# Kernel tuning notes

Hardware: AMD Instinct MI355X
Metric: run time of the kernel (lower is better)

Reference implementation:

```python
import jax, jax.numpy as jnp
import numpy as np

VOCAB, EMB, HID = 50000, 256, 512
H = HID // 2            # per-direction hidden size
K = 24                  # tagset size
START, STOP = 22, 23
B, T = 32, 512
NEG = -10000.0


def setup_inputs():
    key = jax.random.key(0)
    ks = jax.random.split(key, 16)
    s = 0.1  # weight scale to keep gates in a sane range
    sentence = jax.random.randint(ks[0], (B, T), 0, VOCAB)
    embedding = jax.random.normal(ks[1], (VOCAB, EMB), jnp.float32)
    w_ih_f = jax.random.normal(ks[2], (4 * H, EMB), jnp.float32) * s
    w_hh_f = jax.random.normal(ks[3], (4 * H, H), jnp.float32) * s
    b_ih_f = jax.random.normal(ks[4], (4 * H,), jnp.float32) * s
    b_hh_f = jax.random.normal(ks[5], (4 * H,), jnp.float32) * s
    w_ih_b = jax.random.normal(ks[6], (4 * H, EMB), jnp.float32) * s
    w_hh_b = jax.random.normal(ks[7], (4 * H, H), jnp.float32) * s
    b_ih_b = jax.random.normal(ks[8], (4 * H,), jnp.float32) * s
    b_hh_b = jax.random.normal(ks[9], (4 * H,), jnp.float32) * s
    w_out = jax.random.normal(ks[10], (K, HID), jnp.float32) * s
    b_out = jax.random.normal(ks[11], (K,), jnp.float32) * s
    transitions = jax.random.normal(ks[12], (K, K), jnp.float32)
    transitions = transitions.at[START, :].set(NEG).at[:, STOP].set(NEG)
    h0 = jax.random.normal(ks[13], (2, B, H), jnp.float32)  # [fwd,bwd] initial h
    c0 = jax.random.normal(ks[14], (2, B, H), jnp.float32)  # [fwd,bwd] initial c
    return {"sentence": sentence, "embedding": embedding,
            "w_ih_f": w_ih_f, "w_hh_f": w_hh_f, "b_ih_f": b_ih_f, "b_hh_f": b_hh_f,
            "w_ih_b": w_ih_b, "w_hh_b": w_hh_b, "b_ih_b": b_ih_b, "b_hh_b": b_hh_b,
            "w_out": w_out, "b_out": b_out, "transitions": transitions,
            "h0": h0, "c0": c0}


def _lstm_dir(x_tbe, w_ih, w_hh, b_ih, b_hh, h0, c0, reverse):
    # x_tbe: [T, B, E]; PyTorch gate order i, f, g, o
    def step(carry, x_t):
        h, c = carry
        gates = x_t @ w_ih.T + b_ih + h @ w_hh.T + b_hh  # [B, 4H]
        i, f, g, o = jnp.split(gates, 4, axis=-1)
        c = jax.nn.sigmoid(f) * c + jax.nn.sigmoid(i) * jnp.tanh(g)
        h = jax.nn.sigmoid(o) * jnp.tanh(c)
        return (h, c), h
    _, hs = jax.lax.scan(step, (h0, c0), x_tbe, reverse=reverse)
    return hs  # [T, B, H]


def _viterbi(feats_tbk, transitions):
    # feats_tbk: [T, B, K]; transitions[next, prev]
    init = jnp.full((B, K), NEG, feats_tbk.dtype).at[:, START].set(0.0)

    def step(fv, feat_t):
        scores = fv[:, None, :] + transitions[None, :, :]  # [B, next, prev]
        bp = jnp.argmax(scores, axis=-1)                   # [B, K]
        fv_new = jnp.max(scores, axis=-1) + feat_t
        return fv_new, bp

    fv, bps = jax.lax.scan(step, init, feats_tbk)  # bps: [T, B, K]
    terminal = fv + transitions[STOP][None, :]
    last_tag = jnp.argmax(terminal, axis=-1)       # [B]
    path_score = jnp.max(terminal, axis=-1)        # [B]

    def back(tag, bp_t):
        prev = jnp.take_along_axis(bp_t, tag[:, None], axis=1)[:, 0]
        return prev, tag
    # process t = T-1 .. 0; carry holds tag at time t, emits it, steps to t-1
    _, path = jax.lax.scan(back, last_tag, bps, reverse=True)  # [T, B]
    return path_score, path.T.astype(jnp.int32)  # [B], [B, T]


def reference(sentence, embedding, w_ih_f, w_hh_f, b_ih_f, b_hh_f,
              w_ih_b, w_hh_b, b_ih_b, b_hh_b, w_out, b_out,
              transitions, h0, c0):
    emb = embedding[sentence]                       # [B, T, EMB]
    x = jnp.transpose(emb, (1, 0, 2))               # [T, B, EMB]
    hf = _lstm_dir(x, w_ih_f, w_hh_f, b_ih_f, b_hh_f, h0[0], c0[0], False)
    hb = _lstm_dir(x, w_ih_b, w_hh_b, b_ih_b, b_hh_b, h0[1], c0[1], True)
    hs = jnp.concatenate([hf, hb], axis=-1)         # [T, B, HID]
    feats = hs @ w_out.T + b_out                    # [T, B, K]
    score, path = _viterbi(feats, transitions)
    return score, path
```

## Files before the change

kernel.cpp:

```cpp
#include <hip/hip_runtime.h>

#define T_LEN 512
#define BATCH 32
#define HDIR  256
#define KTAG  24
#define START_TAG 22
#define STOP_TAG  23
#define NEGV  (-10000.0f)
#define SENTU 0x7FC0DEADu

typedef float vf4 __attribute__((ext_vector_type(4)));

#define XPROJ_OFF   0ull
#define XPROJ_ELEMS (2ull*512*1024*32)
#define FEATS_OFF   (XPROJ_OFF + XPROJ_ELEMS)
#define FEATS_ELEMS (512ull*32*24)
#define HIST_OFF    (FEATS_OFF + FEATS_ELEMS)
#define HIST_ELEMS  (2ull*513*8192)

#define BARRIER_LGKM() asm volatile("s_waitcnt lgkmcnt(0)\n\ts_barrier" ::: "memory")

__device__ __forceinline__ float fsig(float x) {
  return __builtin_amdgcn_rcpf(1.0f + __expf(-x));
}
__device__ __forceinline__ float ftanh(float x) {
  return 2.0f * __builtin_amdgcn_rcpf(1.0f + __expf(-2.0f * x)) - 1.0f;
}
__device__ __forceinline__ unsigned um(unsigned a, unsigned b) { return a < b ? a : b; }
__device__ __forceinline__ float rdlane(float v, int l) {
  return __uint_as_float((unsigned)__builtin_amdgcn_readlane((int)__float_as_uint(v), l));
}

__global__ void k_fill(float* __restrict__ p, int n4) {
  int i = blockIdx.x * blockDim.x + threadIdx.x;
  if (i < n4) {
    float* dst = p + (size_t)i * 4;
    const float sv = __uint_as_float(SENTU);
    vf4 v; v.x = sv; v.y = sv; v.z = sv; v.w = sv;
    asm volatile("global_store_dwordx4 %0, %1, off sc0 sc1"
                 :: "v"(dst), "v"(v) : "memory");
  }
}

__global__ __launch_bounds__(256, 1) void k_main(
    const int* __restrict__ sent, const float* __restrict__ emb,
    const float* __restrict__ wihf, const float* __restrict__ wihb,
    const float* __restrict__ bihf, const float* __restrict__ bhhf,
    const float* __restrict__ bihb, const float* __restrict__ bhhb,
    const float* __restrict__ whhf, const float* __restrict__ whhb,
    const float* __restrict__ h0, const float* __restrict__ c0,
    const float* __restrict__ wout, const float* __restrict__ bout,
    float* __restrict__ xproj, float* __restrict__ feats,
    float* __restrict__ hist)
{
  extern __shared__ float dynpad[];
  __shared__ float smem[12544];
  const int bid = blockIdx.x;
  const int tid = threadIdx.x;
  if (sent == (const int*)0) dynpad[0] = 0.f;

  if (bid >= 64 && bid < 2112) {
    float (*As)[132] = (float (*)[132])(smem);
    float (*Bs)[132] = (float (*)[132])(smem + 2112);
    int* sid = (int*)(smem + 4224);
    const int idx = bid - 64;
    const int mt_rank = idx >> 4;
    const int sub = idx & 15;
    const int y = sub >> 1;
    const int dir = sub & 1;
    const int mt = (mt_rank & 1) ? (127 - (mt_rank >> 1)) : (mt_rank >> 1);
    const int m0 = mt * 128;
    const int n0 = y * 128;
    const float* __restrict__ W = dir ? wihb : wihf;
    if (tid < 128) {
      int m = m0 + tid;
      sid[tid] = sent[(m & 31) * 512 + (m >> 5)];
    }
    __syncthreads();
    float acc[8][8];
#pragma unroll
    for (int i = 0; i < 8; ++i)
#pragma unroll
      for (int j = 0; j < 8; ++j) acc[i][j] = 0.f;
    const int r = tid >> 1, qq = tid & 1;
    const int ty = tid >> 4, tx = tid & 15;
    const float* ap = &emb[(size_t)sid[r] * 256 + qq * 8];
    const float* bp = &W[(size_t)(n0 + r) * 256 + qq * 8];
    float4 a0 = *(const float4*)(ap);
    float4 a1 = *(const float4*)(ap + 4);
    float4 b0 = *(const float4*)(bp);
    float4 b1 = *(const float4*)(bp + 4);
    for (int k0 = 0; k0 < 256; k0 += 16) {
      __syncthreads();
      As[qq*8+0][r] = a0.x; As[qq*8+1][r] = a0.y; As[qq*8+2][r] = a0.z; As[qq*8+3][r] = a0.w;
      As[qq*8+4][r] = a1.x; As[qq*8+5][r] = a1.y; As[qq*8+6][r] = a1.z; As[qq*8+7][r] = a1.w;
      Bs[qq*8+0][r] = b0.x; Bs[qq*8+1][r] = b0.y; Bs[qq*8+2][r] = b0.z; Bs[qq*8+3][r] = b0.w;
      Bs[qq*8+4][r] = b1.x; Bs[qq*8+5][r] = b1.y; Bs[qq*8+6][r] = b1.z; Bs[qq*8+7][r] = b1.w;
      __syncthreads();
      if (k0 + 16 < 256) {
        const float* ap2 = ap + k0 + 16;
        const float* bp2 = bp + k0 + 16;
        a0 = *(const float4*)(ap2);
        a1 = *(const float4*)(ap2 + 4);
        b0 = *(const float4*)(bp2);
        b1 = *(const float4*)(bp2 + 4);
      }
#pragma unroll
      for (int kk = 0; kk < 16; ++kk) {
        float4 av0 = *(const float4*)&As[kk][ty*8];
        float4 av1 = *(const float4*)&As[kk][ty*8+4];
        float4 bv0 = *(const float4*)&Bs[kk][tx*8];
        float4 bv1 = *(const float4*)&Bs[kk][tx*8+4];
        float am[8] = {av0.x,av0.y,av0.z,av0.w,av1.x,av1.y,av1.z,av1.w};
        float bn[8] = {bv0.x,bv0.y,bv0.z,bv0.w,bv1.x,bv1.y,bv1.z,bv1.w};
#pragma unroll
        for (int i = 0; i < 8; ++i)
#pragma unroll
          for (int j = 0; j < 8; ++j)
            acc[i][j] = fmaf(am[i], bn[j], acc[i][j]);
      }
    }
    const float* bi_p = dir ? bihb : bihf;
    const float* bh_p = dir ? bhhb : bhhf;
    float bias[8];
#pragma unroll
    for (int j = 0; j < 8; ++j) { int n = n0 + tx*8 + j; bias[j] = bi_p[n] + bh_p[n]; }
    const int mb = m0 + ty * 8;
    const int tt = mb >> 5, bb = mb & 31;
#pragma unroll
    for (int j = 0; j < 8; ++j) {
      int n = n0 + tx*8 + j;
      float* dst = &xproj[((((size_t)dir*512 + tt)*1024) + n)*32 + bb];
      vf4 o0, o1;
      o0[0] = acc[0][j]+bias[j]; o0[1] = acc[1][j]+bias[j];
      o0[2] = acc[2][j]+bias[j]; o0[3] = acc[3][j]+bias[j];
      o1[0] = acc[4][j]+bias[j]; o1[1] = acc[5][j]+bias[j];
      o1[2] = acc[6][j]+bias[j]; o1[3] = acc[7][j]+bias[j];
      asm volatile(
        "global_store_dwordx4 %0, %2, off sc0 sc1\n\t"
        "global_store_dwordx4 %1, %3, off sc0 sc1"
        :: "v"(dst), "v"(dst + 4), "v"(o0), "v"(o1) : "memory");
    }
    asm volatile("s_waitcnt vmcnt(0)" ::: "memory");
    __syncthreads();
    if (tid == 0) {
      float* fp = hist + (size_t)dir * 1024 + (size_t)mt * 8 + y;
      const float z = 0.f;
      asm volatile("global_store_dword %0, %1, off sc0 sc1"
                   :: "v"(fp), "v"(z) : "memory");
    }
    return;
  }

  if (bid >= 2112) {
    const int f = bid - 2112;
    const int t = (f & 1) ? (256 + (f >> 1)) : (255 - (f >> 1));
    float* hlds = smem;
    const float* sF = hist + ((size_t)0*513 + (t + 1)) * 8192;
    const float* sB = hist + ((size_t)1*513 + (512 - t)) * 8192;
    {
      const int p = tid & 31;
      const float* pp = (((tid >> 5) & 1) ? sB : sF) + 32 * p;
      while (true) {
        float v;
        asm volatile("global_load_dword %0, %1, off sc0 sc1\n\ts_waitcnt vmcnt(0)"
                     : "=&v"(v) : "v"(pp) : "memory");
        int bad = (__float_as_uint(v) == SENTU) ? 1 : 0;
        if (!__any(bad)) break;
        __builtin_amdgcn_s_sleep(64);
      }
    }
    const int b = tid >> 3, ks = tid & 7;
    float accv[3];
    for (int dir2 = 0; dir2 < 2; ++dir2) {
      const float* sp = (dir2 ? sB : sF) + (size_t)tid * 4;
      vf4 v[8];
      while (true) {
        asm volatile(
          "global_load_dwordx4 %0, %8, off sc0 sc1\n\t"
          "global_load_dwordx4 %1, %9, off sc0 sc1\n\t"
          "global_load_dwordx4 %2, %10, off sc0 sc1\n\t"
          "global_load_dwordx4 %3, %11, off sc0 sc1\n\t"
          "global_load_dwordx4 %4, %12, off sc0 sc1\n\t"
          "global_load_dwordx4 %5, %13, off sc0 sc1\n\t"
          "global_load_dwordx4 %6, %14, off sc0 sc1\n\t"
          "global_load_dwordx4 %7, %15, off sc0 sc1\n\t"
          "s_waitcnt vmcnt(0)"
          : "=&v"(v[0]), "=&v"(v[1]), "=&v"(v[2]), "=&v"(v[3]),
            "=&v"(v[4]), "=&v"(v[5]), "=&v"(v[6]), "=&v"(v[7])
          : "v"(sp), "v"(sp+1024), "v"(sp+2048), "v"(sp+3072),
            "v"(sp+4096), "v"(sp+5120), "v"(sp+6144), "v"(sp+7168)
          : "memory");
        unsigned z = 0xFFFFFFFFu;
#pragma unroll
        for (int q = 0; q < 8; ++q)
#pragma unroll
          for (int bl = 0; bl < 4; ++bl)
            z = um(z, __float_as_uint(v[q][bl]) ^ SENTU);
        if (z) break;
        __builtin_amdgcn_s_sleep(16);
      }
#pragma unroll
      for (int q = 0; q < 8; ++q)
#pragma unroll
        for (int bl = 0; bl < 4; ++bl)
          hlds[(4*q + bl)*258 + tid] = v[q][bl];
      __syncthreads();
#pragma unroll
      for (int kt = 0; kt < 3; ++kt) {
        const int k = kt * 8 + ks;
        if (dir2 == 0) accv[kt] = bout[k];
        const float* wr = wout + (size_t)k * 512 + dir2 * 256;
        float a = accv[kt];
#pragma unroll 8
        for (int kk = 0; kk < 256; kk += 4) {
          float4 h4 = *(const float4*)&hlds[b * 258 + kk];
          float4 w4 = *(const float4*)&wr[kk];
          a += h4.x*w4.x + h4.y*w4.y + h4.z*w4.z + h4.w*w4.w;
        }
        accv[kt] = a;
      }
      __syncthreads();
    }
#pragma unroll
    for (int kt = 0; kt < 3; ++kt)
      feats[((size_t)t * 32 + b) * 24 + kt * 8 + ks] = accv[kt];
    return;
  }

  float* hl = smem + 4352;
  const int dir = bid >> 5;
  const int slice = bid & 31;
  const int rowg = tid >> 5;
  const int bgrp = (tid >> 3) & 3;
  const int kgrp = tid & 7;
  const int jg = slice * 8 + rowg;
  const float* __restrict__ W = dir ? whhb : whhf;

  float2 w2[4][16];
#pragma unroll
  for (int g = 0; g < 4; ++g)
#pragma unroll
    for (int kk2 = 0; kk2 < 16; ++kk2)
      w2[g][kk2] = *(const float2*)&W[(size_t)(g*256 + jg)*256 + kgrp*32 + 2*kk2];

  float cc[8];
#pragma unroll
  for (int bi = 0; bi < 8; ++bi)
    cc[bi] = c0[(size_t)(dir*32 + bgrp*8 + bi)*256 + jg];

  const int kk = tid & 31;
  const int base_col = tid & ~31;
  const int kw4 = 4*((tid >> 5) & 7);
  const int rot = (4*kgrp + 2*bgrp) & 31;
  float* const histd = hist + (size_t)dir * 513 * 8192;
  float hnew[8];

  for (int s = 0; s < 512; ++s) {
    const int t = dir ? (511 - s) : s;

    vf4 hv[8];
    if (s == 0) {
#pragma unroll
      for (int q = 0; q < 8; ++q)
#pragma unroll
        for (int bl = 0; bl < 4; ++bl)
          hv[q][bl] = h0[(size_t)(dir*32 + 4*q + bl)*256 + tid];
    } else {
      const float* sp = histd + (size_t)s*8192 + (size_t)tid*4;
      const float* p0 = sp;
      const float* p1 = sp + 1024;
      const float* p2 = sp + 2048;
      const float* p3 = sp + 3072;
      const float* p4 = sp + 4096;
      const float* p5 = sp + 5120;
      const float* p6 = sp + 6144;
      const float* p7 = sp + 7168;
      while (true) {
        asm volatile(
          "global_load_dwordx4 %0, %1, off sc0 sc1\n\t"
          "s_waitcnt vmcnt(0)"
          : "=&v"(hv[7]) : "v"(p7) : "memory");
        unsigned z = 0xFFFFFFFFu;
#pragma unroll
        for (int bl = 0; bl < 4; ++bl)
          z = um(z, __float_as_uint(hv[7][bl]) ^ SENTU);
        if (z) break;
        __builtin_amdgcn_s_sleep(1);
      }
      while (true) {
        asm volatile(
          "global_load_dwordx4 %0, %7, off sc0 sc1\n\t"
          "global_load_dwordx4 %1, %8, off sc0 sc1\n\t"
          "global_load_dwordx4 %2, %9, off sc0 sc1\n\t"
          "global_load_dwordx4 %3, %10, off sc0 sc1\n\t"
          "global_load_dwordx4 %4, %11, off sc0 sc1\n\t"
          "global_load_dwordx4 %5, %12, off sc0 sc1\n\t"
          "global_load_dwordx4 %6, %13, off sc0 sc1\n\t"
          "s_waitcnt vmcnt(0)"
          : "=&v"(hv[0]), "=&v"(hv[1]), "=&v"(hv[2]), "=&v"(hv[3]),
            "=&v"(hv[4]), "=&v"(hv[5]), "=&v"(hv[6])
          : "v"(p0), "v"(p1), "v"(p2), "v"(p3),
            "v"(p4), "v"(p5), "v"(p6)
          : "memory");
        unsigned z = 0xFFFFFFFFu;
#pragma unroll
        for (int q = 0; q < 7; ++q)
#pragma unroll
          for (int bl = 0; bl < 4; ++bl)
            z = um(z, __float_as_uint(hv[q][bl]) ^ SENTU);
        if (z) break;
        __builtin_amdgcn_s_sleep(1);
      }
    }

    float xpr[4][8];
    if (kgrp == 0) {
      if ((t & 3) == (dir ? 3 : 0)) {
        const float* fp = hist + (size_t)dir*1024 + (size_t)(t >> 2)*8;
        while (true) {
          vf4 f0, f1;
          asm volatile(
            "global_load_dwordx4 %0, %2, off sc0 sc1\n\t"
            "global_load_dwordx4 %1, %3, off sc0 sc1\n\t"
            "s_waitcnt vmcnt(0)"
            : "=&v"(f0), "=&v"(f1) : "v"(fp), "v"(fp + 4) : "memory");
          unsigned bad = 0u;
#pragma unroll
          for (int l = 0; l < 4; ++l) {
            bad |= (__float_as_uint(f0[l]) == SENTU) ? 1u : 0u;
            bad |= (__float_as_uint(f1[l]) == SENTU) ? 1u : 0u;
          }
          if (!bad) break;
          __builtin_amdgcn_s_sleep(2);
        }
      }
#pragma unroll
      for (int g = 0; g < 4; ++g) {
        const float* xp = &xproj[((((size_t)dir*512 + t)*1024) + g*256 + jg)*32 + bgrp*8];
        float4 x0 = *(const float4*)xp;
        float4 x1 = *(const float4*)(xp + 4);
        xpr[g][0]=x0.x; xpr[g][1]=x0.y; xpr[g][2]=x0.z; xpr[g][3]=x0.w;
        xpr[g][4]=x1.x; xpr[g][5]=x1.y; xpr[g][6]=x1.z; xpr[g][7]=x1.w;
      }
    }

#pragma unroll
    for (int q = 0; q < 8; ++q) {
      const int rwq = (kw4 + 2*((q >> 1) & 3)) & 31;
      const int col = base_col + ((kk + rwq) & 31);
#pragma unroll
      for (int bl = 0; bl < 4; ++bl)
        hl[(4*q + bl)*256 + col] = hv[q][bl];
    }
    BARRIER_LGKM();

    float acc[4][8];
#pragma unroll
    for (int g = 0; g < 4; ++g)
#pragma unroll
      for (int bi = 0; bi < 8; ++bi) acc[g][bi] = 0.f;

    const int hbase = kgrp * 32;
#pragma unroll
    for (int kk2 = 0; kk2 < 16; ++kk2) {
      const int idx = hbase + ((2*kk2 + rot) & 31);
      float2 h2[8];
#pragma unroll
      for (int bi = 0; bi < 8; ++bi)
        h2[bi] = *(const float2*)&hl[(bgrp*8 + bi)*256 + idx];
#pragma unroll
      for (int g = 0; g < 4; ++g)
#pragma unroll
        for (int bi = 0; bi < 8; ++bi) {
          acc[g][bi] = fmaf(w2[g][kk2].x, h2[bi].x, acc[g][bi]);
          acc[g][bi] = fmaf(w2[g][kk2].y, h2[bi].y, acc[g][bi]);
        }
    }

    if (kgrp == 0) {
#pragma unroll
      for (int g = 0; g < 4; ++g)
#pragma unroll
        for (int bi = 0; bi < 8; ++bi) acc[g][bi] += xpr[g][bi];
    }
#pragma unroll
    for (int g = 0; g < 4; ++g)
#pragma unroll
      for (int bi = 0; bi < 8; ++bi) {
        float v = acc[g][bi];
        v += __shfl_xor(v, 1, 64);
        v += __shfl_xor(v, 2, 64);
        v += __shfl_xor(v, 4, 64);
        acc[g][bi] = v;
      }

#pragma unroll
    for (int bi = 0; bi < 8; ++bi) {
      float ig = fsig(acc[0][bi]);
      float fg = fsig(acc[1][bi]);
      float gg = ftanh(acc[2][bi]);
      float og = fsig(acc[3][bi]);
      cc[bi] = fg * cc[bi] + ig * gg;
      hnew[bi] = og * ftanh(cc[bi]);
    }

    if (kgrp == 0) {
      float* dp  = histd + (size_t)(s + 1)*8192 + ((size_t)(2*bgrp)*256 + jg)*4;
      float* dp2 = dp + 1024;
      vf4 s0; s0.x = hnew[0]; s0.y = hnew[1]; s0.z = hnew[2]; s0.w = hnew[3];
      vf4 s1; s1.x = hnew[4]; s1.y = hnew[5]; s1.z = hnew[6]; s1.w = hnew[7];
      asm volatile(
        "global_store_dwordx4 %0, %2, off sc0 sc1\n\t"
        "global_store_dwordx4 %1, %3, off sc0 sc1"
        :: "v"(dp), "v"(dp2), "v"(s0), "v"(s1) : "memory");
    }

    BARRIER_LGKM();
  }
}

__global__ __launch_bounds__(64) void k_viterbi(
    const float* __restrict__ feats, const float* __restrict__ trans,
    float* __restrict__ out)
{
  const int b = blockIdx.x;
  const int lane = threadIdx.x;
  __shared__ float fvfin[32];
  __shared__ float pathb[512];
  __shared__ unsigned char bcol[512 * 24];
  float trr[24];
#pragma unroll
  for (int pv = 0; pv < 24; ++pv) trr[pv] = 0.f;
  if (lane < 24) {
#pragma unroll
    for (int pv = 0; pv < 24; ++pv) trr[pv] = trans[lane * 24 + pv];
  }
  float fv = (lane == START_TAG) ? 0.f : NEGV;
  float fcur = (lane < 24) ? feats[b * 24 + lane] : 0.f;
  for (int t = 0; t < 512; ++t) {
    float fnext = (t < 511 && lane < 24) ? feats[(size_t)(t + 1) * 768 + b * 24 + lane] : 0.f;
    float s[24];
#pragma unroll
    for (int pv = 0; pv < 24; ++pv) s[pv] = rdlane(fv, pv);
    float c0v = -3.4e38f, c1v = -3.4e38f, c2v = -3.4e38f, c3v = -3.4e38f;
    int   c0i = 0, c1i = 6, c2i = 12, c3i = 18;
#pragma unroll
    for (int j = 0; j < 6; ++j) {
      float v0 = s[j]      + trr[j];
      float v1 = s[6 + j]  + trr[6 + j];
      float v2 = s[12 + j] + trr[12 + j];
      float v3 = s[18 + j] + trr[18 + j];
      if (v0 > c0v) { c0v = v0; c0i = j; }
      if (v1 > c1v) { c1v = v1; c1i = 6 + j; }
      if (v2 > c2v) { c2v = v2; c2i = 12 + j; }
      if (v3 > c3v) { c3v = v3; c3i = 18 + j; }
    }
    if (c1v > c0v) { c0v = c1v; c0i = c1i; }
    if (c3v > c2v) { c2v = c3v; c2i = c3i; }
    float best = c0v; int bp = c0i;
    if (c2v > best) { best = c2v; bp = c2i; }
    if (lane < 24) bcol[t * 24 + lane] = (unsigned char)bp;
    fv = best + fcur;
    fcur = fnext;
  }
  if (lane < 32) fvfin[lane] = (lane < 24) ? fv : NEGV;
  __syncthreads();
  if (lane == 0) {
    float best = -3.4e38f; int bt = 0;
#pragma unroll
    for (int kk2 = 0; kk2 < 24; ++kk2) {
      float v = fvfin[kk2] + trans[STOP_TAG * 24 + kk2];
      if (v > best) { best = v; bt = kk2; }
    }
    out[b] = best;
    pathb[511] = (float)bt;
    int tag = bt;
    for (int t = 511; t >= 1; --t) {
      tag = bcol[t * 24 + tag];
      pathb[t - 1] = (float)tag;
    }
  }
  __syncthreads();
#pragma unroll
  for (int it = 0; it < 8; ++it)
    out[32 + (size_t)b * 512 + it * 64 + lane] = pathb[it * 64 + lane];
}

extern "C" void kernel_launch(void* const* d_in, const int* in_sizes, int n_in,
                              void* d_out, int out_size, void* d_ws, size_t ws_size,
                              hipStream_t stream) {
  (void)in_sizes; (void)n_in; (void)out_size; (void)ws_size;
  const int*   sent = (const int*)d_in[0];
  const float* emb  = (const float*)d_in[1];
  const float* wihf = (const float*)d_in[2];
  const float* whhf = (const float*)d_in[3];
  const float* bihf = (const float*)d_in[4];
  const float* bhhf = (const float*)d_in[5];
  const float* wihb = (const float*)d_in[6];
  const float* whhb = (const float*)d_in[7];
  const float* bihb = (const float*)d_in[8];
  const float* bhhb = (const float*)d_in[9];
  const float* wout = (const float*)d_in[10];
  const float* bout = (const float*)d_in[11];
  const float* trans= (const float*)d_in[12];
  const float* h0   = (const float*)d_in[13];
  const float* c0   = (const float*)d_in[14];

  float* ws     = (float*)d_ws;
  float* xproj  = ws + XPROJ_OFF;
  float* feats  = ws + FEATS_OFF;
  float* hist   = ws + HIST_OFF;

  const int n4 = (int)(HIST_ELEMS / 4);
  k_fill<<<(n4 + 255) / 256, 256, 0, stream>>>(hist, n4);
  k_main<<<2624, 256, 32768, stream>>>(sent, emb, wihf, wihb,
                                       bihf, bhhf, bihb, bhhb,
                                       whhf, whhb, h0, c0,
                                       wout, bout, xproj, feats, hist);
  k_viterbi<<<32, 64, 0, stream>>>(feats, trans, (float*)d_out);
}
```

Before: 4.095 ms.

## Interleave forward and backward LSTM directions in one set of recurrent blocks

The recurrent part used to run 64 persistent blocks, 32 per direction. It now runs 32 blocks, and each block alternates a forward step and a backward step. Forward W_hh stays in registers, while backward W_hh is held in dynamic LDS with a rotated layout. The hidden-state loads for the other direction are issued as prefetches before the current direction's compute, so global-memory latency is overlapped with the other direction's work. This halves the number of cross-block sync participants per step and frees CUs for the projection GEMM. The cost is serialising two directions per block and adding LDS reads of the backward weights on the critical path.

```diff
diff --git a/kernel.cpp b/kernel.cpp
--- a/kernel.cpp
+++ b/kernel.cpp
@@ -54,16 +54,15 @@
     float* __restrict__ hist)
 {
   extern __shared__ float dynpad[];
-  __shared__ float smem[12544];
+  __shared__ float smem[8256];
   const int bid = blockIdx.x;
   const int tid = threadIdx.x;
-  if (sent == (const int*)0) dynpad[0] = 0.f;
-
-  if (bid >= 64 && bid < 2112) {
+
+  if (bid >= 32 && bid < 2080) {
     float (*As)[132] = (float (*)[132])(smem);
     float (*Bs)[132] = (float (*)[132])(smem + 2112);
     int* sid = (int*)(smem + 4224);
-    const int idx = bid - 64;
+    const int idx = bid - 32;
     const int mt_rank = idx >> 4;
     const int sub = idx & 15;
     const int y = sub >> 1;
@@ -152,8 +151,8 @@
     return;
   }
 
-  if (bid >= 2112) {
-    const int f = bid - 2112;
+  if (bid >= 2080) {
+    const int f = bid - 2080;
     const int t = (f & 1) ? (256 + (f >> 1)) : (255 - (f >> 1));
     float* hlds = smem;
     const float* sF = hist + ((size_t)0*513 + (t + 1)) * 8192;
@@ -228,96 +227,124 @@
     return;
   }
 
-  float* hl = smem + 4352;
-  const int dir = bid >> 5;
-  const int slice = bid & 31;
+  float* hl   = smem;
+  float* wlds = dynpad;
+  const int slice = bid;
   const int rowg = tid >> 5;
   const int bgrp = (tid >> 3) & 3;
   const int kgrp = tid & 7;
   const int jg = slice * 8 + rowg;
-  const float* __restrict__ W = dir ? whhb : whhf;
 
   float2 w2[4][16];
 #pragma unroll
   for (int g = 0; g < 4; ++g)
 #pragma unroll
     for (int kk2 = 0; kk2 < 16; ++kk2)
-      w2[g][kk2] = *(const float2*)&W[(size_t)(g*256 + jg)*256 + kgrp*32 + 2*kk2];
-
-  float cc[8];
-#pragma unroll
-  for (int bi = 0; bi < 8; ++bi)
-    cc[bi] = c0[(size_t)(dir*32 + bgrp*8 + bi)*256 + jg];
+      w2[g][kk2] = *(const float2*)&whhf[(size_t)(g*256 + jg)*256 + kgrp*32 + 2*kk2];
+
+  {
+    const int g = bgrp;
+    const int rotw_s = (4*kgrp + 2*rowg) & 31;
+    const float* srcw = &whhb[(size_t)(g*256 + jg)*256 + kgrp*32];
+    float* dstw = &wlds[(g*8 + rowg)*256 + kgrp*32];
+    for (int off = 0; off < 32; ++off)
+      dstw[off] = srcw[(off - rotw_s + 32) & 31];
+  }
+
+  float ccf[8], ccb[8];
+#pragma unroll
+  for (int bi = 0; bi < 8; ++bi) {
+    ccf[bi] = c0[(size_t)(bgrp*8 + bi)*256 + jg];
+    ccb[bi] = c0[(size_t)(32 + bgrp*8 + bi)*256 + jg];
+  }
 
   const int kk = tid & 31;
   const int base_col = tid & ~31;
   const int kw4 = 4*((tid >> 5) & 7);
   const int rot = (4*kgrp + 2*bgrp) & 31;
-  float* const histd = hist + (size_t)dir * 513 * 8192;
+  const int rotw = (4*kgrp + 2*rowg) & 31;
+  float* const hist0 = hist;
+  float* const hist1 = hist + (size_t)513 * 8192;
   float hnew[8];
+  vf4 hv[8];
+  __syncthreads();
 
   for (int s = 0; s < 512; ++s) {
-    const int t = dir ? (511 - s) : s;
-
-    vf4 hv[8];
     if (s == 0) {
 #pragma unroll
       for (int q = 0; q < 8; ++q)
 #pragma unroll
         for (int bl = 0; bl < 4; ++bl)
-          hv[q][bl] = h0[(size_t)(dir*32 + 4*q + bl)*256 + tid];
+          hv[q][bl] = h0[(size_t)(4*q + bl)*256 + tid];
     } else {
-      const float* sp = histd + (size_t)s*8192 + (size_t)tid*4;
-      const float* p0 = sp;
-      const float* p1 = sp + 1024;
-      const float* p2 = sp + 2048;
-      const float* p3 = sp + 3072;
-      const float* p4 = sp + 4096;
-      const float* p5 = sp + 5120;
-      const float* p6 = sp + 6144;
-      const float* p7 = sp + 7168;
-      while (true) {
+      const float* sp = hist0 + (size_t)s*8192 + (size_t)tid*4;
+      asm volatile("s_waitcnt vmcnt(0)"
+                   : "+v"(hv[0]), "+v"(hv[1]), "+v"(hv[2]), "+v"(hv[3]),
+                     "+v"(hv[4]), "+v"(hv[5]), "+v"(hv[6]), "+v"(hv[7])
+                   :: "memory");
+      unsigned z = 0xFFFFFFFFu;
+#pragma unroll
+      for (int q = 0; q < 8; ++q)
+#pragma unroll
+        for (int bl = 0; bl < 4; ++bl)
+          z = um(z, __float_as_uint(hv[q][bl]) ^ SENTU);
+      while (!z) {
+        __builtin_amdgcn_s_sleep(1);
         asm volatile(
-          "global_load_dwordx4 %0, %1, off sc0 sc1\n\t"
-          "s_waitcnt vmcnt(0)"
-          : "=&v"(hv[7]) : "v"(p7) : "memory");
-        unsigned z = 0xFFFFFFFFu;
-#pragma unroll
-        for (int bl = 0; bl < 4; ++bl)
-          z = um(z, __float_as_uint(hv[7][bl]) ^ SENTU);
-        if (z) break;
-        __builtin_amdgcn_s_sleep(1);
-      }
-      while (true) {
-        asm volatile(
-          "global_load_dwordx4 %0, %7, off sc0 sc1\n\t"
-          "global_load_dwordx4 %1, %8, off sc0 sc1\n\t"
-          "global_load_dwordx4 %2, %9, off sc0 sc1\n\t"
-          "global_load_dwordx4 %3, %10, off sc0 sc1\n\t"
-          "global_load_dwordx4 %4, %11, off sc0 sc1\n\t"
-          "global_load_dwordx4 %5, %12, off sc0 sc1\n\t"
-          "global_load_dwordx4 %6, %13, off sc0 sc1\n\t"
+          "global_load_dwordx4 %0, %8, off sc0 sc1\n\t"
+          "global_load_dwordx4 %1, %9, off sc0 sc1\n\t"
+          "global_load_dwordx4 %2, %10, off sc0 sc1\n\t"
+          "global_load_dwordx4 %3, %11, off sc0 sc1\n\t"
+          "global_load_dwordx4 %4, %12, off sc0 sc1\n\t"
+          "global_load_dwordx4 %5, %13, off sc0 sc1\n\t"
+          "global_load_dwordx4 %6, %14, off sc0 sc1\n\t"
+          "global_load_dwordx4 %7, %15, off sc0 sc1\n\t"
           "s_waitcnt vmcnt(0)"
           : "=&v"(hv[0]), "=&v"(hv[1]), "=&v"(hv[2]), "=&v"(hv[3]),
-            "=&v"(hv[4]), "=&v"(hv[5]), "=&v"(hv[6])
-          : "v"(p0), "v"(p1), "v"(p2), "v"(p3),
-            "v"(p4), "v"(p5), "v"(p6)
+            "=&v"(hv[4]), "=&v"(hv[5]), "=&v"(hv[6]), "=&v"(hv[7])
+          : "v"(sp), "v"(sp+1024), "v"(sp+2048), "v"(sp+3072),
+            "v"(sp+4096), "v"(sp+5120), "v"(sp+6144), "v"(sp+7168)
           : "memory");
-        unsigned z = 0xFFFFFFFFu;
-#pragma unroll
-        for (int q = 0; q < 7; ++q)
+        z = 0xFFFFFFFFu;
+#pragma unroll
+        for (int q = 0; q < 8; ++q)
 #pragma unroll
           for (int bl = 0; bl < 4; ++bl)
             z = um(z, __float_as_uint(hv[q][bl]) ^ SENTU);
-        if (z) break;
-        __builtin_amdgcn_s_sleep(1);
-      }
+      }
+    }
+
+#pragma unroll
+    for (int q = 0; q < 8; ++q) {
+      const int rwq = (kw4 + 2*((q >> 1) & 3)) & 31;
+      const int col = base_col + ((kk + rwq) & 31);
+#pragma unroll
+      for (int bl = 0; bl < 4; ++bl)
+        hl[(4*q + bl)*256 + col] = hv[q][bl];
+    }
+
+    if (s >= 1) {
+      const float* sb = hist1 + (size_t)s*8192 + (size_t)tid*4;
+      asm volatile(
+        "global_load_dwordx4 %0, %8, off sc0 sc1\n\t"
+        "global_load_dwordx4 %1, %9, off sc0 sc1\n\t"
+        "global_load_dwordx4 %2, %10, off sc0 sc1\n\t"
+        "global_load_dwordx4 %3, %11, off sc0 sc1\n\t"
+        "global_load_dwordx4 %4, %12, off sc0 sc1\n\t"
+        "global_load_dwordx4 %5, %13, off sc0 sc1\n\t"
+        "global_load_dwordx4 %6, %14, off sc0 sc1\n\t"
+        "global_load_dwordx4 %7, %15, off sc0 sc1"
+        : "=&v"(hv[0]), "=&v"(hv[1]), "=&v"(hv[2]), "=&v"(hv[3]),
+          "=&v"(hv[4]), "=&v"(hv[5]), "=&v"(hv[6]), "=&v"(hv[7])
+        : "v"(sb), "v"(sb+1024), "v"(sb+2048), "v"(sb+3072),
+          "v"(sb+4096), "v"(sb+5120), "v"(sb+6144), "v"(sb+7168)
+        : "memory");
     }
 
     float xpr[4][8];
     if (kgrp == 0) {
-      if ((t & 3) == (dir ? 3 : 0)) {
-        const float* fp = hist + (size_t)dir*1024 + (size_t)(t >> 2)*8;
+      if ((s & 3) == 0) {
+        const float* fp = hist + (size_t)(s >> 2)*8;
         while (true) {
           vf4 f0, f1;
           asm volatile(
@@ -337,22 +364,13 @@
       }
 #pragma unroll
       for (int g = 0; g < 4; ++g) {
-        const float* xp = &xproj[((((size_t)dir*512 + t)*1024) + g*256 + jg)*32 + bgrp*8];
+        const float* xp = &xproj[(((size_t)s*1024) + g*256 + jg)*32 + bgrp*8];
         float4 x0 = *(const float4*)xp;
         float4 x1 = *(const float4*)(xp + 4);
         xpr[g][0]=x0.x; xpr[g][1]=x0.y; xpr[g][2]=x0.z; xpr[g][3]=x0.w;
         xpr[g][4]=x1.x; xpr[g][5]=x1.y; xpr[g][6]=x1.z; xpr[g][7]=x1.w;
       }
     }
-
-#pragma unroll
-    for (int q = 0; q < 8; ++q) {
-      const int rwq = (kw4 + 2*((q >> 1) & 3)) & 31;
-      const int col = base_col + ((kk + rwq) & 31);
-#pragma unroll
-      for (int bl = 0; bl < 4; ++bl)
-        hl[(4*q + bl)*256 + col] = hv[q][bl];
-    }
     BARRIER_LGKM();
 
     float acc[4][8];
@@ -360,7 +378,6 @@
     for (int g = 0; g < 4; ++g)
 #pragma unroll
       for (int bi = 0; bi < 8; ++bi) acc[g][bi] = 0.f;
-
     const int hbase = kgrp * 32;
 #pragma unroll
     for (int kk2 = 0; kk2 < 16; ++kk2) {
@@ -377,7 +394,6 @@
           acc[g][bi] = fmaf(w2[g][kk2].y, h2[bi].y, acc[g][bi]);
         }
     }
-
     if (kgrp == 0) {
 #pragma unroll
       for (int g = 0; g < 4; ++g)
@@ -394,19 +410,17 @@
         v += __shfl_xor(v, 4, 64);
         acc[g][bi] = v;
       }
-
 #pragma unroll
     for (int bi = 0; bi < 8; ++bi) {
       float ig = fsig(acc[0][bi]);
       float fg = fsig(acc[1][bi]);
       float gg = ftanh(acc[2][bi]);
       float og = fsig(acc[3][bi]);
-      cc[bi] = fg * cc[bi] + ig * gg;
-      hnew[bi] = og * ftanh(cc[bi]);
-    }
-
+      ccf[bi] = fg * ccf[bi] + ig * gg;
+      hnew[bi] = og * ftanh(ccf[bi]);
+    }
     if (kgrp == 0) {
-      float* dp  = histd + (size_t)(s + 1)*8192 + ((size_t)(2*bgrp)*256 + jg)*4;
+      float* dp  = hist0 + (size_t)(s + 1)*8192 + ((size_t)(2*bgrp)*256 + jg)*4;
       float* dp2 = dp + 1024;
       vf4 s0; s0.x = hnew[0]; s0.y = hnew[1]; s0.z = hnew[2]; s0.w = hnew[3];
       vf4 s1; s1.x = hnew[4]; s1.y = hnew[5]; s1.z = hnew[6]; s1.w = hnew[7];
@@ -415,7 +429,185 @@
         "global_store_dwordx4 %1, %3, off sc0 sc1"
         :: "v"(dp), "v"(dp2), "v"(s0), "v"(s1) : "memory");
     }
-
+    BARRIER_LGKM();
+
+    const int tb = 511 - s;
+    if (s == 0) {
+#pragma unroll
+      for (int q = 0; q < 8; ++q)
+#pragma unroll
+        for (int bl = 0; bl < 4; ++bl)
+          hv[q][bl] = h0[(size_t)(32 + 4*q + bl)*256 + tid];
+      asm volatile("s_waitcnt vmcnt(0)" ::: "memory");
+    } else {
+      const float* sp = hist1 + (size_t)s*8192 + (size_t)tid*4;
+      asm volatile("s_waitcnt vmcnt(0)"
+                   : "+v"(hv[0]), "+v"(hv[1]), "+v"(hv[2]), "+v"(hv[3]),
+                     "+v"(hv[4]), "+v"(hv[5]), "+v"(hv[6]), "+v"(hv[7])
+                   :: "memory");
+      unsigned z = 0xFFFFFFFFu;
+#pragma unroll
+      for (int q = 0; q < 8; ++q)
+#pragma unroll
+        for (int bl = 0; bl < 4; ++bl)
+          z = um(z, __float_as_uint(hv[q][bl]) ^ SENTU);
+      while (!z) {
+        __builtin_amdgcn_s_sleep(1);
+        asm volatile(
+          "global_load_dwordx4 %0, %8, off sc0 sc1\n\t"
+          "global_load_dwordx4 %1, %9, off sc0 sc1\n\t"
+          "global_load_dwordx4 %2, %10, off sc0 sc1\n\t"
+          "global_load_dwordx4 %3, %11, off sc0 sc1\n\t"
+          "global_load_dwordx4 %4, %12, off sc0 sc1\n\t"
+          "global_load_dwordx4 %5, %13, off sc0 sc1\n\t"
+          "global_load_dwordx4 %6, %14, off sc0 sc1\n\t"
+          "global_load_dwordx4 %7, %15, off sc0 sc1\n\t"
+          "s_waitcnt vmcnt(0)"
+          : "=&v"(hv[0]), "=&v"(hv[1]), "=&v"(hv[2]), "=&v"(hv[3]),
+            "=&v"(hv[4]), "=&v"(hv[5]), "=&v"(hv[6]), "=&v"(hv[7])
+          : "v"(sp), "v"(sp+1024), "v"(sp+2048), "v"(sp+3072),
+            "v"(sp+4096), "v"(sp+5120), "v"(sp+6144), "v"(sp+7168)
+          : "memory");
+        z = 0xFFFFFFFFu;
+#pragma unroll
+        for (int q = 0; q < 8; ++q)
+#pragma unroll
+          for (int bl = 0; bl < 4; ++bl)
+            z = um(z, __float_as_uint(hv[q][bl]) ^ SENTU);
+      }
+    }
+
+#pragma unroll
+    for (int q = 0; q < 8; ++q) {
+      const int rwq = (kw4 + 2*((q >> 1) & 3)) & 31;
+      const int col = base_col + ((kk + rwq) & 31);
+#pragma unroll
+      for (int bl = 0; bl < 4; ++bl)
+        hl[(4*q + bl)*256 + col] = hv[q][bl];
+    }
+
+    if (s < 511) {
+      const float* sf = hist0 + (size_t)(s + 1)*8192 + (size_t)tid*4;
+      asm volatile(
+        "global_load_dwordx4 %0, %8, off sc0 sc1\n\t"
+        "global_load_dwordx4 %1, %9, off sc0 sc1\n\t"
+        "global_load_dwordx4 %2, %10, off sc0 sc1\n\t"
+        "global_load_dwordx4 %3, %11, off sc0 sc1\n\t"
+        "global_load_dwordx4 %4, %12, off sc0 sc1\n\t"
+        "global_load_dwordx4 %5, %13, off sc0 sc1\n\t"
+        "global_load_dwordx4 %6, %14, off sc0 sc1\n\t"
+        "global_load_dwordx4 %7, %15, off sc0 sc1"
+        : "=&v"(hv[0]), "=&v"(hv[1]), "=&v"(hv[2]), "=&v"(hv[3]),
+          "=&v"(hv[4]), "=&v"(hv[5]), "=&v"(hv[6]), "=&v"(hv[7])
+        : "v"(sf), "v"(sf+1024), "v"(sf+2048), "v"(sf+3072),
+          "v"(sf+4096), "v"(sf+5120), "v"(sf+6144), "v"(sf+7168)
+        : "memory");
+    }
+
+    if (kgrp == 0) {
+      if ((tb & 3) == 3) {
+        const float* fp = hist + 1024 + (size_t)(tb >> 2)*8;
+        while (true) {
+          vf4 f0, f1;
+          asm volatile(
+            "global_load_dwordx4 %0, %2, off sc0 sc1\n\t"
+            "global_load_dwordx4 %1, %3, off sc0 sc1\n\t"
+            "s_waitcnt vmcnt(0)"
+            : "=&v"(f0), "=&v"(f1) : "v"(fp), "v"(fp + 4) : "memory");
+          unsigned bad = 0u;
+#pragma unroll
+          for (int l = 0; l < 4; ++l) {
+            bad |= (__float_as_uint(f0[l]) == SENTU) ? 1u : 0u;
+            bad |= (__float_as_uint(f1[l]) == SENTU) ? 1u : 0u;
+          }
+          if (!bad) break;
+          __builtin_amdgcn_s_sleep(2);
+        }
+      }
+#pragma unroll
+      for (int g = 0; g < 4; ++g) {
+        const float* xp = &xproj[(((size_t)(512 + tb)*1024) + g*256 + jg)*32 + bgrp*8];
+        float4 x0 = *(const float4*)xp;
+        float4 x1 = *(const float4*)(xp + 4);
+        xpr[g][0]=x0.x; xpr[g][1]=x0.y; xpr[g][2]=x0.z; xpr[g][3]=x0.w;
+        xpr[g][4]=x1.x; xpr[g][5]=x1.y; xpr[g][6]=x1.z; xpr[g][7]=x1.w;
+      }
+    }
+    BARRIER_LGKM();
+
+#pragma unroll
+    for (int g = 0; g < 4; ++g)
+#pragma unroll
+      for (int bi = 0; bi < 8; ++bi) acc[g][bi] = 0.f;
+    const float* wbB = &wlds[rowg*256 + kgrp*32];
+#pragma unroll
+    for (int kk2 = 0; kk2 < 16; ++kk2) {
+      const int wo = (2*kk2 + rotw) & 31;
+      float2 wv0 = *(const float2*)&wbB[0*2048 + wo];
+      float2 wv1 = *(const float2*)&wbB[1*2048 + wo];
+      float2 wv2 = *(const float2*)&wbB[2*2048 + wo];
+      float2 wv3 = *(const float2*)&wbB[3*2048 + wo];
+      const int idx = hbase + ((2*kk2 + rot) & 31);
+      float2 h2[8];
+#pragma unroll
+      for (int bi = 0; bi < 8; ++bi)
+        h2[bi] = *(const float2*)&hl[(bgrp*8 + bi)*256 + idx];
+#pragma unroll
+      for (int bi = 0; bi < 8; ++bi) {
+        acc[0][bi] = fmaf(wv0.x, h2[bi].x, acc[0][bi]);
+        acc[0][bi] = fmaf(wv0.y, h2[bi].y, acc[0][bi]);
+      }
+#pragma unroll
+      for (int bi = 0; bi < 8; ++bi) {
+        acc[1][bi] = fmaf(wv1.x, h2[bi].x, acc[1][bi]);
+        acc[1][bi] = fmaf(wv1.y, h2[bi].y, acc[1][bi]);
+      }
+#pragma unroll
+      for (int bi = 0; bi < 8; ++bi) {
+        acc[2][bi] = fmaf(wv2.x, h2[bi].x, acc[2][bi]);
+        acc[2][bi] = fmaf(wv2.y, h2[bi].y, acc[2][bi]);
+      }
+#pragma unroll
+      for (int bi = 0; bi < 8; ++bi) {
+        acc[3][bi] = fmaf(wv3.x, h2[bi].x, acc[3][bi]);
+        acc[3][bi] = fmaf(wv3.y, h2[bi].y, acc[3][bi]);
+      }
+    }
+    if (kgrp == 0) {
+#pragma unroll
+      for (int g = 0; g < 4; ++g)
+#pragma unroll
+        for (int bi = 0; bi < 8; ++bi) acc[g][bi] += xpr[g][bi];
+    }
+#pragma unroll
+    for (int g = 0; g < 4; ++g)
+#pragma unroll
+      for (int bi = 0; bi < 8; ++bi) {
+        float v = acc[g][bi];
+        v += __shfl_xor(v, 1, 64);
+        v += __shfl_xor(v, 2, 64);
+        v += __shfl_xor(v, 4, 64);
+        acc[g][bi] = v;
+      }
+#pragma unroll
+    for (int bi = 0; bi < 8; ++bi) {
+      float ig = fsig(acc[0][bi]);
+      float fg = fsig(acc[1][bi]);
+      float gg = ftanh(acc[2][bi]);
+      float og = fsig(acc[3][bi]);
+      ccb[bi] = fg * ccb[bi] + ig * gg;
+      hnew[bi] = og * ftanh(ccb[bi]);
+    }
+    if (kgrp == 0) {
+      float* dp  = hist1 + (size_t)(s + 1)*8192 + ((size_t)(2*bgrp)*256 + jg)*4;
+      float* dp2 = dp + 1024;
+      vf4 s0; s0.x = hnew[0]; s0.y = hnew[1]; s0.z = hnew[2]; s0.w = hnew[3];
+      vf4 s1; s1.x = hnew[4]; s1.y = hnew[5]; s1.z = hnew[6]; s1.w = hnew[7];
+      asm volatile(
+        "global_store_dwordx4 %0, %2, off sc0 sc1\n\t"
+        "global_store_dwordx4 %1, %3, off sc0 sc1"
+        :: "v"(dp), "v"(dp2), "v"(s0), "v"(s1) : "memory");
+    }
     BARRIER_LGKM();
   }
 }
@@ -514,7 +706,7 @@
 
   const int n4 = (int)(HIST_ELEMS / 4);
   k_fill<<<(n4 + 255) / 256, 256, 0, stream>>>(hist, n4);
-  k_main<<<2624, 256, 32768, stream>>>(sent, emb, wihf, wihb,
+  k_main<<<2592, 256, 49152, stream>>>(sent, emb, wihf, wihb,
                                        bihf, bhhf, bihb, bhhb,
                                        whhf, whhb, h0, c0,
                                        wout, bout, xproj, feats, hist);
```

Result: slower. 8.867 ms (+116.5%).
